# Optimization experiments

Measured on AMD Instinct MI355X. Metric: run time of the kernel, lower is better.

The kernel has to match this reference:

```python
import jax, jax.numpy as jnp
import numpy as np
from jax import lax

NMS_THRESH = 0.5
BN_EPS = 1e-5
TO_REMOVE = 1.0  # neural-motifs box convention (+1 in width/height)


def nms_overlaps(boxes):
    # boxes: [N, C, 4] xyxy -> per-class pairwise IoU [N, N, C]
    x1 = jnp.maximum(boxes[:, None, :, 0], boxes[None, :, :, 0])
    y1 = jnp.maximum(boxes[:, None, :, 1], boxes[None, :, :, 1])
    x2 = jnp.minimum(boxes[:, None, :, 2], boxes[None, :, :, 2])
    y2 = jnp.minimum(boxes[:, None, :, 3], boxes[None, :, :, 3])
    inter = jnp.clip(x2 - x1 + TO_REMOVE, 0.0) * jnp.clip(y2 - y1 + TO_REMOVE, 0.0)
    area = (boxes[:, :, 2] - boxes[:, :, 0] + TO_REMOVE) * (boxes[:, :, 3] - boxes[:, :, 1] + TO_REMOVE)  # [N,C]
    union = area[:, None, :] + area[None, :, :] - inter
    return inter / union


def greedy_nms_labels(obj_dists, is_overlap):
    # faithful port of nms_per_cls: iterative argmax + per-class suppression
    N, C = obj_dists.shape
    scores = jax.nn.softmax(obj_dists, axis=-1)
    scores = scores.at[:, 0].set(-1.0)  # kill background column

    def step(carry, _):
        scores, labels = carry
        flat = jnp.argmax(scores)          # row-major, same as np.unravel_index
        box_ind = flat // C
        cls_ind = flat % C
        labels = labels.at[box_ind].set(cls_ind.astype(jnp.int32))
        ov = is_overlap[box_ind, :, cls_ind]  # [N] bool
        col = jnp.where(ov, 0.0, scores[:, cls_ind])
        scores = scores.at[:, cls_ind].set(col)
        scores = scores.at[box_ind, :].set(-1.0)
        return (scores, labels), None

    (_, labels), _ = lax.scan(step, (scores, jnp.zeros(N, jnp.int32)), None, length=N)
    return labels


def setup_inputs() -> dict:
    key = jax.random.key(0)
    ks = jax.random.split(key, 16)
    N, C, D, E, H, P = 400, 151, 4096, 200, 512, 128
    x = jax.random.normal(ks[0], (N, D), jnp.float32)
    predict_logits = jax.random.normal(ks[1], (N, C), jnp.float32) * 2.0
    pos_input = jax.random.uniform(ks[2], (N, 9), jnp.float32)
    xy = jax.random.uniform(ks[3], (N, C, 2), jnp.float32) * 800.0
    wh = jax.random.uniform(ks[4], (N, C, 2), jnp.float32) * 200.0 + 1.0
    boxes_per_cls = jnp.concatenate([xy, xy + wh], axis=-1)
    sc = lambda k, sh: jax.random.normal(k, sh, jnp.float32) * np.float32(1.0 / np.sqrt(sh[0]))
    return {
        'x': x,
        'predict_logits': predict_logits,
        'pos_input': pos_input,
        'boxes_per_cls': boxes_per_cls,
        'obj_embed_w': jax.random.normal(ks[5], (C, E), jnp.float32) * 0.1,
        'obj_embed2_w': jax.random.normal(ks[6], (C, E), jnp.float32) * 0.1,
        'w_pos1': sc(ks[7], (9, 32)), 'b_pos1': jnp.zeros(32, jnp.float32),
        'bn_gamma': jnp.ones(32, jnp.float32), 'bn_beta': jnp.zeros(32, jnp.float32),
        'bn_mean': jnp.zeros(32, jnp.float32), 'bn_var': jnp.ones(32, jnp.float32),
        'w_pos2': sc(ks[8], (32, P)), 'b_pos2': jnp.zeros(P, jnp.float32),
        'w_lin': sc(ks[9], (D + E + P, H)), 'b_lin': jnp.zeros(H, jnp.float32),
        'w_out': sc(ks[10], (H, C)), 'b_out': jnp.zeros(C, jnp.float32),
        'w_fc': sc(ks[11], (D + E + P, H)), 'b_fc': jnp.zeros(H, jnp.float32),
    }


def reference(x, predict_logits, pos_input, boxes_per_cls, obj_embed_w, obj_embed2_w,
              w_pos1, b_pos1, bn_gamma, bn_beta, bn_mean, bn_var, w_pos2, b_pos2,
              w_lin, b_lin, w_out, b_out, w_fc, b_fc):
    # sgdet inference path of VTransEFeaturePE.forward
    obj_embed = jax.nn.softmax(predict_logits, axis=-1) @ obj_embed_w           # [N,E]
    h = pos_input @ w_pos1 + b_pos1                                             # Linear(9,32)
    h = (h - bn_mean) / jnp.sqrt(bn_var + BN_EPS) * bn_gamma + bn_beta          # BN eval
    pos_embed = jax.nn.relu(h @ w_pos2 + b_pos2)                                # [N,128]
    rep = jnp.concatenate([x, obj_embed, pos_embed], axis=-1)                   # [N,4424]
    obj_dists = (rep @ w_lin + b_lin) @ w_out + b_out                           # [N,C]
    is_overlap = nms_overlaps(boxes_per_cls) >= NMS_THRESH                      # [N,N,C]
    obj_preds = greedy_nms_labels(obj_dists, is_overlap)                        # [N] int32
    obj_embed2 = obj_embed2_w[obj_preds]                                        # [N,E]
    obj_rel_rep = jnp.concatenate([x, pos_embed, obj_embed2], axis=-1)
    edge_ctx = jax.nn.relu(obj_rel_rep @ w_fc + b_fc)                           # [N,H]
    return (obj_dists, obj_preds, edge_ctx)
```

## Files before the change

### kernel.cpp

```cpp
#include <hip/hip_runtime.h>
#include <hip/hip_bf16.h>
#include <stdint.h>

#define NB 400
#define NC 151
#define DX 4096
#define DE 200
#define DP 128
#define DH 512
#define KREP 4424
#define TAILW 328
#define MPAD 416
#define SPLITK 8
#define TILES1 139
#define TILES2 132
#define SKSTRIDE 152

__device__ __forceinline__ uint32_t f2ord(float f) {
  uint32_t u = __float_as_uint(f);
  return (u & 0x80000000u) ? ~u : (u | 0x80000000u);
}

__global__ __launch_bounds__(256) void k_embed(
    const float* __restrict__ logits, const float* __restrict__ obj_embed_w,
    const float* __restrict__ pos_input, const float* __restrict__ w_pos1,
    const float* __restrict__ b_pos1, const float* __restrict__ bn_gamma,
    const float* __restrict__ bn_beta, const float* __restrict__ bn_mean,
    const float* __restrict__ bn_var, const float* __restrict__ w_pos2,
    const float* __restrict__ b_pos2, float* __restrict__ tail1) {
  int r = blockIdx.x, t = threadIdx.x;
  if (r >= NB) {
    if (t < TAILW) tail1[r * TAILW + t] = 0.f;
    return;
  }
  __shared__ float p[NC];
  __shared__ float red[256];
  __shared__ float hb[32];

  float v = (t < NC) ? logits[r * NC + t] : -INFINITY;
  red[t] = v; __syncthreads();
  for (int s = 128; s > 0; s >>= 1) { if (t < s) red[t] = fmaxf(red[t], red[t + s]); __syncthreads(); }
  float m = red[0]; __syncthreads();
  float e = (t < NC) ? expf(v - m) : 0.f;
  red[t] = e; __syncthreads();
  for (int s = 128; s > 0; s >>= 1) { if (t < s) red[t] += red[t + s]; __syncthreads(); }
  float sum = red[0];
  if (t < NC) p[t] = e / sum;

  if (t < 32) {
    float acc = b_pos1[t];
    for (int k = 0; k < 9; k++) acc += pos_input[r * 9 + k] * w_pos1[k * 32 + t];
    acc = (acc - bn_mean[t]) / sqrtf(bn_var[t] + 1e-5f) * bn_gamma[t] + bn_beta[t];
    hb[t] = acc;
  }
  __syncthreads();

  if (t < DE) {
    float acc = 0.f;
    for (int k = 0; k < NC; k++) acc += p[k] * obj_embed_w[k * DE + t];
    tail1[r * TAILW + t] = acc;
  }
  if (t < DP) {
    float acc = b_pos2[t];
    for (int k = 0; k < 32; k++) acc += hb[k] * w_pos2[k * DP + t];
    tail1[r * TAILW + DE + t] = fmaxf(acc, 0.f);
  }
}

__device__ __forceinline__ void gemm_body(
    float (*As)[36], float (*Bs)[68],
    const float* __restrict__ x, const float* __restrict__ tail,
    const float* __restrict__ w, float* __restrict__ part,
    int bid, int tiles, int toff) {
  int tid = threadIdx.x;
  int n0 = (bid & 7) * 64, m0 = ((bid >> 3) % 13) * 32;
  int z = bid / 104;
  int tbeg = (z * tiles) / SPLITK, tend = ((z + 1) * tiles) / SPLITK;
  int ty = tid >> 4, tx = tid & 15;
  int a_r = tid >> 3, a_c = (tid & 7) << 2;
  int b_r = tid >> 4, b_c = (tid & 15) << 2;
  float4 acc0 = {0, 0, 0, 0}, acc1 = {0, 0, 0, 0};

  auto loadA = [&](int t) -> float4 {
    int k = t * 32 + a_c;
    int row = m0 + a_r;
    float4 v = {0, 0, 0, 0};
    if (k < KREP) {
      if (k < DX) { if (row < NB) v = *(const float4*)&x[(size_t)row * DX + k]; }
      else v = *(const float4*)&tail[row * TAILW + toff + (k - DX)];
    }
    return v;
  };
  auto loadB = [&](int t, int roff) -> float4 {
    int k = t * 32 + b_r + roff;
    float4 v = {0, 0, 0, 0};
    if (k < KREP) v = *(const float4*)&w[(size_t)k * DH + n0 + b_c];
    return v;
  };

  float4 pa = loadA(tbeg), pb0 = loadB(tbeg, 0), pb1 = loadB(tbeg, 16);
  for (int t = tbeg; t < tend; t++) {
    __syncthreads();
    *(float4*)&As[a_r][a_c] = pa;
    *(float4*)&Bs[b_r][b_c] = pb0;
    *(float4*)&Bs[b_r + 16][b_c] = pb1;
    __syncthreads();
    if (t + 1 < tend) { pa = loadA(t + 1); pb0 = loadB(t + 1, 0); pb1 = loadB(t + 1, 16); }
#pragma unroll
    for (int k4 = 0; k4 < 8; k4++) {
      float4 a0 = *(float4*)&As[ty * 2][k4 * 4];
      float4 a1 = *(float4*)&As[ty * 2 + 1][k4 * 4];
#pragma unroll
      for (int j = 0; j < 4; j++) {
        float4 bv = *(float4*)&Bs[k4 * 4 + j][tx * 4];
        float av0 = (&a0.x)[j], av1 = (&a1.x)[j];
        acc0.x += av0 * bv.x; acc0.y += av0 * bv.y; acc0.z += av0 * bv.z; acc0.w += av0 * bv.w;
        acc1.x += av1 * bv.x; acc1.y += av1 * bv.y; acc1.z += av1 * bv.z; acc1.w += av1 * bv.w;
      }
    }
  }
  int row0 = m0 + ty * 2, col = n0 + tx * 4;
  float* base = part + (size_t)z * NB * DH;
  if (row0 < NB)     *(float4*)&base[row0 * DH + col] = acc0;
  if (row0 + 1 < NB) *(float4*)&base[(row0 + 1) * DH + col] = acc1;
}

__global__ __launch_bounds__(256) void k_g1ov(
    const float* __restrict__ x, const float* __restrict__ tail1,
    const float* __restrict__ w_lin, float* __restrict__ part,
    const float* __restrict__ boxes, uint64_t* __restrict__ ov_bits) {
  __shared__ __align__(16) float As[32][36];
  __shared__ __align__(16) float Bs[32][68];
  int bid = blockIdx.x;
  if (bid >= 832) {
    int c = bid - 832;
    int t = threadIdx.x;
    __shared__ float4 bx[NB];
    const float4* bp4 = (const float4*)boxes;
    for (int j = t; j < NB; j += 256) bx[j] = bp4[j * NC + c];
    __syncthreads();
    int wave = t >> 6, lane = t & 63;
    for (int b = wave; b < NB; b += 4) {
      float4 A = bx[b];
      float areaA = (A.z - A.x + 1.f) * (A.w - A.y + 1.f);
      for (int chunk = 0; chunk < 7; chunk++) {
        int j = chunk * 64 + lane;
        bool ov = false;
        if (j < NB) {
          float4 B = bx[j];
          float x1 = fmaxf(A.x, B.x), y1 = fmaxf(A.y, B.y);
          float x2 = fminf(A.z, B.z), y2 = fminf(A.w, B.w);
          float iw = fmaxf(x2 - x1 + 1.f, 0.f), ih = fmaxf(y2 - y1 + 1.f, 0.f);
          float inter = iw * ih;
          float areaB = (B.z - B.x + 1.f) * (B.w - B.y + 1.f);
          ov = (inter / (areaA + areaB - inter)) >= 0.5f;
        }
        uint64_t mask = __ballot(ov);
        if (lane == 0) ov_bits[((size_t)(b * NC + c) << 3) + chunk] = mask;
      }
    }
    return;
  }
  gemm_body(As, Bs, x, tail1, w_lin, part, bid, TILES1, 0);
}

__global__ __launch_bounds__(256) void k_dists(
    const float* __restrict__ part, const float* __restrict__ b_lin,
    const float* __restrict__ w_out, const float* __restrict__ b_out,
    float* __restrict__ out_dists, uint64_t* __restrict__ skeys) {
  int r = blockIdx.x, t = threadIdx.x;
  __shared__ float h[DH];
  __shared__ float red[256];
  __shared__ float sval[NC];
  float s0 = b_lin[t], s1 = b_lin[t + 256];
#pragma unroll
  for (int z = 0; z < SPLITK; z++) {
    const float* pr = part + ((size_t)z * NB + r) * DH;
    s0 += pr[t]; s1 += pr[t + 256];
  }
  h[t] = s0; h[t + 256] = s1;
  __syncthreads();

  float acc = -INFINITY;
  if (t < NC) {
    acc = b_out[t];
    for (int k = 0; k < DH; k++) acc += h[k] * w_out[k * NC + t];
    out_dists[r * NC + t] = acc;
  }
  red[t] = (t < NC) ? acc : -INFINITY; __syncthreads();
  for (int s = 128; s > 0; s >>= 1) { if (t < s) red[t] = fmaxf(red[t], red[t + s]); __syncthreads(); }
  float mx = red[0]; __syncthreads();
  float e = (t < NC) ? expf(acc - mx) : 0.f;
  red[t] = e; __syncthreads();
  for (int s = 128; s > 0; s >>= 1) { if (t < s) red[t] += red[t + s]; __syncthreads(); }
  float sum = red[0];
  if (t < NC) sval[t] = e / sum;
  __syncthreads();

  if (t >= 1 && t < NC) {
    float v = sval[t];
    int rank = 0;
    for (int c2 = 1; c2 < NC; c2++) {
      float v2 = sval[c2];
      rank += (v2 > v) || (v2 == v && c2 < t);
    }
    skeys[(size_t)r * SKSTRIDE + rank] =
        ((uint64_t)f2ord(v) << 17) | ((uint64_t)(511 - r) << 8) | (uint64_t)t;
  }
}

struct GemmSm { float As[32][36]; float Bs[32][68]; };
struct NmsSm  { uint64_t top4[2][4][4]; uint64_t amask[8]; uint64_t rmask[8];
                uint8_t rcol[512]; };

__global__ __launch_bounds__(256) void k_nms_g2a(
    const uint64_t* __restrict__ ov_bits, const uint64_t* __restrict__ skeys,
    int* __restrict__ labels_g, float* __restrict__ out_preds,
    const float* __restrict__ x, const float* __restrict__ tail1,
    const float* __restrict__ w_fc, float* __restrict__ part) {
  __shared__ __align__(16) union { GemmSm g; NmsSm n; } sm;
  if (blockIdx.x > 0) {
    gemm_body(sm.g.As, sm.g.Bs, x, tail1, w_fc, part, blockIdx.x - 1, TILES2, DE);
    return;
  }
  int tid = threadIdx.x, wave = tid >> 6, lane = tid & 63;
  int S0w = wave * 2;
  uint64_t cand[2];
  uint64_t supp0[2], supp1[2], supp2[2];
  int depth[2];
  bool removed[2];
  int reszmin[2];

#pragma unroll
  for (int u = 0; u < 2; u++) {
    int r = (S0w + u) * 64 + lane;
    supp0[u] = supp1[u] = supp2[u] = 0;
    depth[u] = 0; removed[u] = false; reszmin[u] = 255;
    if (r < NB) {
      cand[u] = skeys[(size_t)r * SKSTRIDE];
      labels_g[r] = 0; out_preds[r] = 0.f;
    } else cand[u] = 0;
  }

  auto cswap = [](uint64_t& a, uint64_t& b) {
    uint64_t hi = a > b ? a : b, lo = a > b ? b : a; a = hi; b = lo;
  };

  int picked = 0, rr = 0;
  while (picked < NB) {
    int pp = rr & 1; rr++;
    uint64_t k0 = cand[0] > cand[1] ? cand[0] : cand[1];
    uint64_t k1 = cand[0] > cand[1] ? cand[1] : cand[0];
    uint64_t k2 = 0, k3 = 0;
#pragma unroll
    for (int off = 1; off < 64; off <<= 1) {
      uint64_t p0 = (uint64_t)__shfl_xor((unsigned long long)k0, off, 64);
      uint64_t p1 = (uint64_t)__shfl_xor((unsigned long long)k1, off, 64);
      uint64_t p2 = (uint64_t)__shfl_xor((unsigned long long)k2, off, 64);
      uint64_t p3 = (uint64_t)__shfl_xor((unsigned long long)k3, off, 64);
      uint64_t t0 = k0 > p3 ? k0 : p3;
      uint64_t t1 = k1 > p2 ? k1 : p2;
      uint64_t t2 = k2 > p1 ? k2 : p1;
      uint64_t t3 = k3 > p0 ? k3 : p0;
      cswap(t0, t2); cswap(t1, t3); cswap(t0, t1); cswap(t2, t3);
      k0 = t0; k1 = t1; k2 = t2; k3 = t3;
    }
    if (lane < 4) {
      uint64_t kv = (lane == 0) ? k0 : (lane == 1) ? k1 : (lane == 2) ? k2 : k3;
      sm.n.top4[pp][wave][lane] = kv;
    }
    __syncthreads();

    uint64_t A0 = sm.n.top4[pp][0][0], A1 = sm.n.top4[pp][0][1], A2 = sm.n.top4[pp][0][2], A3 = sm.n.top4[pp][0][3];
    uint64_t B0 = sm.n.top4[pp][1][0], B1 = sm.n.top4[pp][1][1], B2 = sm.n.top4[pp][1][2], B3 = sm.n.top4[pp][1][3];
    uint64_t C0 = sm.n.top4[pp][2][0], C1 = sm.n.top4[pp][2][1], C2 = sm.n.top4[pp][2][2], C3 = sm.n.top4[pp][2][3];
    uint64_t D0 = sm.n.top4[pp][3][0], D1 = sm.n.top4[pp][3][1], D2 = sm.n.top4[pp][3][2], D3 = sm.n.top4[pp][3][3];
    uint64_t x0 = A0, x1 = A1, x2 = A2, x3 = A3, x4 = B3, x5 = B2, x6 = B1, x7 = B0;
    cswap(x0,x4); cswap(x1,x5); cswap(x2,x6); cswap(x3,x7);
    cswap(x0,x2); cswap(x1,x3); cswap(x4,x6); cswap(x5,x7);
    cswap(x0,x1); cswap(x2,x3); cswap(x4,x5); cswap(x6,x7);
    uint64_t y0 = C0, y1 = C1, y2 = C2, y3 = C3, y4 = D3, y5 = D2, y6 = D1, y7 = D0;
    cswap(y0,y4); cswap(y1,y5); cswap(y2,y6); cswap(y3,y7);
    cswap(y0,y2); cswap(y1,y3); cswap(y4,y6); cswap(y5,y7);
    cswap(y0,y1); cswap(y2,y3); cswap(y4,y5); cswap(y6,y7);
    uint64_t tk[8];
    tk[0] = x0 > y7 ? x0 : y7;  tk[1] = x1 > y6 ? x1 : y6;
    tk[2] = x2 > y5 ? x2 : y5;  tk[3] = x3 > y4 ? x3 : y4;
    tk[4] = x4 > y3 ? x4 : y3;  tk[5] = x5 > y2 ? x5 : y2;
    tk[6] = x6 > y1 ? x6 : y1;  tk[7] = x7 > y0 ? x7 : y0;
    cswap(tk[0],tk[4]); cswap(tk[1],tk[5]); cswap(tk[2],tk[6]); cswap(tk[3],tk[7]);
    cswap(tk[0],tk[2]); cswap(tk[1],tk[3]); cswap(tk[4],tk[6]); cswap(tk[5],tk[7]);
    cswap(tk[0],tk[1]); cswap(tk[2],tk[3]); cswap(tk[4],tk[5]); cswap(tk[6],tk[7]);

    if ((uint32_t)(tk[0] >> 17) <= 0x80000000u) break;

    int cntA = 0, cntB = 0, cntC = 0, cntD = 0;
#pragma unroll
    for (int i = 0; i < 8; i++) {
      cntA += (tk[i] > A3); cntB += (tk[i] > B3);
      cntC += (tk[i] > C3); cntD += (tk[i] > D3);
    }
    int mincnt = cntA < cntB ? cntA : cntB;
    mincnt = mincnt < cntC ? mincnt : cntC;
    mincnt = mincnt < cntD ? mincnt : cntD;

    int npick = NB - picked; if (npick > 8) npick = 8;

    int pi = lane >> 3, pw = lane & 7;
    int bsel = 0, csel = 0;
#pragma unroll
    for (int i = 0; i < 8; i++)
      if (pi == i) {
        bsel = 511 - (int)((tk[i] >> 8) & 0x1FF);
        csel = (int)(tk[i] & 0xFF);
      }
    uint64_t wv = 0;
    if (pi < npick && pw < 7)
      wv = ov_bits[(((size_t)(bsel * NC + csel)) << 3) + pw];
    uint32_t packed = ((uint32_t)bsel << 8) | (uint32_t)csel;

    uint64_t balnz_raw = __ballot(wv != 0ull);

    uint64_t ovall = 0;
#pragma unroll
    for (int j = 0; j < 8; j++) {
      int bj = 511 - (int)((tk[j] >> 8) & 0x1FF);
      bool hit = (pw == (bj >> 6)) && ((wv >> (bj & 63)) & 1);
      uint64_t bal = __ballot(hit);
      bal |= bal >> 4; bal |= bal >> 2; bal |= bal >> 1;
      uint32_t m8 = (uint32_t)(((bal & 0x0101010101010101ULL) * 0x0102040810204080ULL) >> 56);
      ovall |= (uint64_t)m8 << (8 * j);
    }

    int napply = 1; bool stop = false;
#pragma unroll
    for (int j = 1; j < 8; j++) {
      bool bad = (j >= npick) || (j > mincnt) ||
                 ((uint32_t)(tk[j] >> 17) <= 0x80000000u);
      int cjv = (int)(tk[j] & 0xFF);
#pragma unroll
      for (int i = 0; i < j; i++)
        bad = bad || (((int)(tk[i] & 0xFF) == cjv) && ((ovall >> (8 * j + i)) & 1));
      stop = stop || bad;
      if (!stop) napply = j + 1;
    }

    uint64_t am = (napply >= 8) ? ~0ull : ((1ull << (8 * napply)) - 1);
    uint64_t balnz = balnz_raw & am;

#pragma unroll
    for (int u = 0; u < 2; u++) {
      int S = S0w + u;
      int r = S * 64 + lane;
      for (int i = 0; i < napply; i++) {
        int bc = __shfl((int)packed, i * 8, 64);
        int b = (bc >> 8) & 0x1FF, c = bc & 0xFF;
        bool act = ((balnz >> (i * 8 + S)) & 1) || ((b >> 6) == S);
        if (!act) continue;
        uint64_t owv = (uint64_t)__shfl((unsigned long long)wv, i * 8 + S, 64);
        if (r == b) {
          removed[u] = true; reszmin[u] = 255;
          cand[u] = ((uint64_t)0x407FFFFFu << 17) | ((uint64_t)(511 - r) << 8);
          labels_g[b] = c; out_preds[b] = (float)c;
        } else if ((owv >> lane) & 1) {
          if (removed[u]) {
            if (c < reszmin[u]) reszmin[u] = c;
            cand[u] = ((uint64_t)0x80000000u << 17) | ((uint64_t)(511 - r) << 8)
                      | (uint64_t)reszmin[u];
          } else {
            uint64_t bit = 1ull << (c & 63);
            if (c < 64) supp0[u] |= bit; else if (c < 128) supp1[u] |= bit; else supp2[u] |= bit;
            if ((int)(cand[u] & 0xFF) == c) {
              int d = depth[u] + 1;
              uint64_t k = 0;
              for (; d < 150; d++) {
                k = skeys[(size_t)r * SKSTRIDE + d];
                int col = (int)(k & 0xFF);
                uint64_t mm = (col < 64) ? supp0[u] : ((col < 128) ? supp1[u] : supp2[u]);
                if (!((mm >> (col & 63)) & 1)) break;
              }
              if (d >= 150)
                k = ((uint64_t)0x80000000u << 17) | ((uint64_t)(511 - r) << 8) | 1ull;
              depth[u] = d; cand[u] = k;
            }
          }
        }
      }
    }
    picked += napply;
  }

  if (picked < NB) {
#pragma unroll
    for (int u = 0; u < 2; u++) {
      int r = (S0w + u) * 64 + lane;
      uint64_t am = __ballot(r < NB && !removed[u]);
      uint64_t rm = __ballot(removed[u] &&
                             (uint32_t)(cand[u] >> 17) == 0x80000000u);
      sm.n.rcol[(S0w + u) * 64 + lane] = (uint8_t)reszmin[u];
      if (lane == 0) { sm.n.amask[S0w + u] = am; sm.n.rmask[S0w + u] = rm; }
    }
    __syncthreads();
    if (wave != 0) return;

    uint64_t A[8], R[8];
    uint32_t rc[8];
#pragma unroll
    for (int s = 0; s < 8; s++) {
      A[s] = sm.n.amask[s];
      R[s] = sm.n.rmask[s];
      rc[s] = sm.n.rcol[s * 64 + lane];
    }

    while (picked < NB) {
      int b = 0, sstar = 0; bool found = false;
#pragma unroll
      for (int s = 0; s < 8; s++) {
        uint64_t cm = A[s] | R[s];
        if (!found && cm != 0ull) {
          found = true; sstar = s;
          b = s * 64 + (int)__builtin_ctzll(cm);
        }
      }
      bool fromA = false;
      uint32_t colv = 0;
      if (found) {
#pragma unroll
        for (int s = 0; s < 8; s++)
          if (s == sstar) fromA = (A[s] >> (b & 63)) & 1ull;
        if (fromA) colv = 1;
        else {
          uint32_t cv = 0;
#pragma unroll
          for (int s = 0; s < 8; s++) {
            uint32_t v = (uint32_t)__shfl((int)rc[s], b & 63, 64);
            if (s == sstar) cv = v;
          }
          colv = cv;
        }
      }
      uint64_t w = 0;
      if (lane < 7) w = ov_bits[(((size_t)(b * NC + (int)colv)) << 3) + lane];
      uint64_t W[8];
#pragma unroll
      for (int s = 0; s < 8; s++)
        W[s] = (uint64_t)__shfl((unsigned long long)w, s, 64);
      uint64_t T[8];
#pragma unroll
      for (int s = 0; s < 8; s++) {
        uint64_t valid = (s < 6) ? ~0ull : ((s == 6) ? 0xFFFFull : 0ull);
        T[s] = W[s] & valid & ~A[s];
      }
#pragma unroll
      for (int s = 0; s < 8; s++)
        if (s == sstar) T[s] &= ~(1ull << (b & 63));
#pragma unroll
      for (int s = 0; s < 8; s++)
        if (s == sstar) {
          if (fromA) A[s] &= ~(1ull << (b & 63));
          else       R[s] &= ~(1ull << (b & 63));
        }
#pragma unroll
      for (int s = 0; s < 8; s++) {
        R[s] |= T[s];
        if ((T[s] >> lane) & 1ull) rc[s] = rc[s] < colv ? rc[s] : colv;
      }
      if (!fromA) {
#pragma unroll
        for (int s = 0; s < 8; s++)
          if (s == sstar && lane == (b & 63)) rc[s] = 255;
      }
      if (lane == 0) { labels_g[b] = (int)colv; out_preds[b] = (float)colv; }
      picked++;
    }
  }
}

__global__ __launch_bounds__(256) void k_final(
    const float* __restrict__ emb2, const int* __restrict__ labels,
    const float* __restrict__ w_fc, const float* __restrict__ part,
    const float* __restrict__ b_fc, float* __restrict__ out_edge) {
  __shared__ __align__(16) float As[32][36];
  __shared__ __align__(16) float Bs[32][68];
  int tid = threadIdx.x;
  int n0 = blockIdx.x * 64, m0 = blockIdx.y * 32;
  int ty = tid >> 4, tx = tid & 15;
  int a_r = tid >> 3, a_c = (tid & 7) << 2;
  int b_r = tid >> 4, b_c = (tid & 15) << 2;
  float4 acc0 = {0, 0, 0, 0}, acc1 = {0, 0, 0, 0};
  int row_a = m0 + a_r;
  int lab = (row_a < NB) ? labels[row_a] : 0;

  auto loadA = [&](int t) -> float4 {
    int kk = t * 32 + a_c;
    float4 v = {0, 0, 0, 0};
    if (kk < DE && row_a < NB) v = *(const float4*)&emb2[(size_t)lab * DE + kk];
    return v;
  };
  auto loadB = [&](int t, int roff) -> float4 {
    int kk = t * 32 + b_r + roff;
    float4 v = {0, 0, 0, 0};
    if (kk < DE) v = *(const float4*)&w_fc[(size_t)(DX + DP + kk) * DH + n0 + b_c];
    return v;
  };

  float4 pa = loadA(0), pb0 = loadB(0, 0), pb1 = loadB(0, 16);
  for (int t = 0; t < 7; t++) {
    __syncthreads();
    *(float4*)&As[a_r][a_c] = pa;
    *(float4*)&Bs[b_r][b_c] = pb0;
    *(float4*)&Bs[b_r + 16][b_c] = pb1;
    __syncthreads();
    if (t + 1 < 7) { pa = loadA(t + 1); pb0 = loadB(t + 1, 0); pb1 = loadB(t + 1, 16); }
#pragma unroll
    for (int k4 = 0; k4 < 8; k4++) {
      float4 a0 = *(float4*)&As[ty * 2][k4 * 4];
      float4 a1 = *(float4*)&As[ty * 2 + 1][k4 * 4];
#pragma unroll
      for (int j = 0; j < 4; j++) {
        float4 bv = *(float4*)&Bs[k4 * 4 + j][tx * 4];
        float av0 = (&a0.x)[j], av1 = (&a1.x)[j];
        acc0.x += av0 * bv.x; acc0.y += av0 * bv.y; acc0.z += av0 * bv.z; acc0.w += av0 * bv.w;
        acc1.x += av1 * bv.x; acc1.y += av1 * bv.y; acc1.z += av1 * bv.z; acc1.w += av1 * bv.w;
      }
    }
  }
  int row0 = m0 + ty * 2, col = n0 + tx * 4;
#pragma unroll
  for (int z = 0; z < SPLITK; z++) {
    if (row0 < NB) {
      float4 p = *(const float4*)&part[((size_t)z * NB + row0) * DH + col];
      acc0.x += p.x; acc0.y += p.y; acc0.z += p.z; acc0.w += p.w;
    }
    if (row0 + 1 < NB) {
      float4 p = *(const float4*)&part[((size_t)z * NB + row0 + 1) * DH + col];
      acc1.x += p.x; acc1.y += p.y; acc1.z += p.z; acc1.w += p.w;
    }
  }
  float4 bv = *(const float4*)&b_fc[col];
  if (row0 < NB) {
    float4 r;
    r.x = fmaxf(acc0.x + bv.x, 0.f); r.y = fmaxf(acc0.y + bv.y, 0.f);
    r.z = fmaxf(acc0.z + bv.z, 0.f); r.w = fmaxf(acc0.w + bv.w, 0.f);
    *(float4*)&out_edge[row0 * DH + col] = r;
  }
  if (row0 + 1 < NB) {
    float4 r;
    r.x = fmaxf(acc1.x + bv.x, 0.f); r.y = fmaxf(acc1.y + bv.y, 0.f);
    r.z = fmaxf(acc1.z + bv.z, 0.f); r.w = fmaxf(acc1.w + bv.w, 0.f);
    *(float4*)&out_edge[(row0 + 1) * DH + col] = r;
  }
}

extern "C" void kernel_launch(void* const* d_in, const int* in_sizes, int n_in,
                              void* d_out, int out_size, void* d_ws, size_t ws_size,
                              hipStream_t stream) {
  const float* x            = (const float*)d_in[0];
  const float* logits       = (const float*)d_in[1];
  const float* pos_input    = (const float*)d_in[2];
  const float* boxes        = (const float*)d_in[3];
  const float* obj_embed_w  = (const float*)d_in[4];
  const float* obj_embed2_w = (const float*)d_in[5];
  const float* w_pos1       = (const float*)d_in[6];
  const float* b_pos1       = (const float*)d_in[7];
  const float* bn_gamma     = (const float*)d_in[8];
  const float* bn_beta      = (const float*)d_in[9];
  const float* bn_mean      = (const float*)d_in[10];
  const float* bn_var       = (const float*)d_in[11];
  const float* w_pos2       = (const float*)d_in[12];
  const float* b_pos2       = (const float*)d_in[13];
  const float* w_lin        = (const float*)d_in[14];
  const float* b_lin        = (const float*)d_in[15];
  const float* w_out        = (const float*)d_in[16];
  const float* b_out        = (const float*)d_in[17];
  const float* w_fc         = (const float*)d_in[18];
  const float* b_fc         = (const float*)d_in[19];

  float* ws         = (float*)d_ws;
  float* tail1      = ws;
  int* labels       = (int*)(tail1 + MPAD * TAILW);
  uint64_t* skeys   = (uint64_t*)(labels + MPAD);
  uint64_t* ov_bits = skeys + (size_t)NB * SKSTRIDE;
  float* part       = (float*)(ov_bits + (size_t)NB * NC * 8);

  float* out       = (float*)d_out;
  float* out_dists = out;
  float* out_preds = out + NB * NC;
  float* out_edge  = out + NB * NC + NB;

  k_embed<<<MPAD, 256, 0, stream>>>(logits, obj_embed_w, pos_input, w_pos1, b_pos1,
                                    bn_gamma, bn_beta, bn_mean, bn_var, w_pos2, b_pos2,
                                    tail1);
  k_g1ov<<<983, 256, 0, stream>>>(x, tail1, w_lin, part, boxes, ov_bits);
  k_dists<<<NB, 256, 0, stream>>>(part, b_lin, w_out, b_out, out_dists, skeys);
  k_nms_g2a<<<833, 256, 0, stream>>>(ov_bits, skeys, labels, out_preds,
                                     x, tail1, w_fc, part);
  k_final<<<dim3(8, 13), 256, 0, stream>>>(obj_embed2_w, labels, w_fc, part,
                                           b_fc, out_edge);
}
```

Measured before the change: 566.5 us.

## Cache per-row overlap bitmasks in LDS for the serial NMS tail

Before the single-wave serial tail loop, the block preloads each remaining row's overlap bitmask row into shared memory, using class 1 or the row's recorded min suppressed class. The per-pick global load on the serial critical path becomes an LDS read. When a row's recorded class drops, its cached mask is refreshed from global memory inside the loop, per suppressed bit. This adds about 25KB of shared memory to the union and serial per-bit work, which may lower occupancy of the GEMM blocks sharing the kernel.

Result: no change. 567.5 us (+0.2%).

```diff
diff --git a/kernel.cpp b/kernel.cpp
--- a/kernel.cpp
+++ b/kernel.cpp
@@ -211,7 +211,7 @@
 
 struct GemmSm { float As[32][36]; float Bs[32][68]; };
 struct NmsSm  { uint64_t top4[2][4][4]; uint64_t amask[8]; uint64_t rmask[8];
-                uint8_t rcol[512]; };
+                uint32_t rcol32[512]; uint64_t ovc[NB][8]; };
 
 __global__ __launch_bounds__(256) void k_nms_g2a(
     const uint64_t* __restrict__ ov_bits, const uint64_t* __restrict__ skeys,
@@ -397,20 +397,28 @@
       uint64_t am = __ballot(r < NB && !removed[u]);
       uint64_t rm = __ballot(removed[u] &&
                              (uint32_t)(cand[u] >> 17) == 0x80000000u);
-      sm.n.rcol[(S0w + u) * 64 + lane] = (uint8_t)reszmin[u];
+      sm.n.rcol32[(S0w + u) * 64 + lane] = (uint32_t)reszmin[u];
       if (lane == 0) { sm.n.amask[S0w + u] = am; sm.n.rmask[S0w + u] = rm; }
     }
     __syncthreads();
+    for (int i = tid; i < NB * 8; i += 256) {
+      int r = i >> 3, w = i & 7;
+      sm.n.ovc[r][w] = (w < 7) ? ov_bits[(((size_t)(r * NC + 1)) << 3) + w] : 0;
+    }
+    __syncthreads();
+    for (int r = tid; r < NB; r += 256) {
+      if ((sm.n.rmask[r >> 6] >> (r & 63)) & 1ull) {
+        uint32_t c = sm.n.rcol32[r];
+        for (int w = 0; w < 7; w++)
+          sm.n.ovc[r][w] = ov_bits[(((size_t)(r * NC + (int)c)) << 3) + w];
+      }
+    }
+    __syncthreads();
     if (wave != 0) return;
 
     uint64_t A[8], R[8];
-    uint32_t rc[8];
-#pragma unroll
-    for (int s = 0; s < 8; s++) {
-      A[s] = sm.n.amask[s];
-      R[s] = sm.n.rmask[s];
-      rc[s] = sm.n.rcol[s * 64 + lane];
-    }
+#pragma unroll
+    for (int s = 0; s < 8; s++) { A[s] = sm.n.amask[s]; R[s] = sm.n.rmask[s]; }
 
     while (picked < NB) {
       int b = 0, sstar = 0; bool found = false;
@@ -423,28 +431,25 @@
         }
       }
       bool fromA = false;
+#pragma unroll
+      for (int s = 0; s < 8; s++)
+        if (s == sstar) fromA = (A[s] >> (b & 63)) & 1ull;
+      if (!found) fromA = false;
       uint32_t colv = 0;
+      if (found) colv = fromA ? 1u : sm.n.rcol32[b];
+
+      uint64_t W[8];
       if (found) {
 #pragma unroll
+        for (int s = 0; s < 7; s++) W[s] = sm.n.ovc[b][s];
+        W[7] = 0;
+      } else {
+        uint64_t w = 0;
+        if (lane < 7) w = ov_bits[(((size_t)(b * NC + (int)colv)) << 3) + lane];
+#pragma unroll
         for (int s = 0; s < 8; s++)
-          if (s == sstar) fromA = (A[s] >> (b & 63)) & 1ull;
-        if (fromA) colv = 1;
-        else {
-          uint32_t cv = 0;
-#pragma unroll
-          for (int s = 0; s < 8; s++) {
-            uint32_t v = (uint32_t)__shfl((int)rc[s], b & 63, 64);
-            if (s == sstar) cv = v;
-          }
-          colv = cv;
-        }
-      }
-      uint64_t w = 0;
-      if (lane < 7) w = ov_bits[(((size_t)(b * NC + (int)colv)) << 3) + lane];
-      uint64_t W[8];
-#pragma unroll
-      for (int s = 0; s < 8; s++)
-        W[s] = (uint64_t)__shfl((unsigned long long)w, s, 64);
+          W[s] = (uint64_t)__shfl((unsigned long long)w, s, 64);
+      }
       uint64_t T[8];
 #pragma unroll
       for (int s = 0; s < 8; s++) {
@@ -453,22 +458,35 @@
       }
 #pragma unroll
       for (int s = 0; s < 8; s++)
-        if (s == sstar) T[s] &= ~(1ull << (b & 63));
-#pragma unroll
-      for (int s = 0; s < 8; s++)
         if (s == sstar) {
-          if (fromA) A[s] &= ~(1ull << (b & 63));
-          else       R[s] &= ~(1ull << (b & 63));
+          T[s] &= ~(1ull << (b & 63));
+          if (found) {
+            if (fromA) A[s] &= ~(1ull << (b & 63));
+            else       R[s] &= ~(1ull << (b & 63));
+          }
         }
+      if (found && !fromA) {
+        if (lane == 0) sm.n.rcol32[b] = 255;
+      }
+#pragma unroll
+      for (int s = 0; s < 8; s++) R[s] |= T[s];
+
 #pragma unroll
       for (int s = 0; s < 8; s++) {
-        R[s] |= T[s];
-        if ((T[s] >> lane) & 1ull) rc[s] = rc[s] < colv ? rc[s] : colv;
-      }
-      if (!fromA) {
-#pragma unroll
-        for (int s = 0; s < 8; s++)
-          if (s == sstar && lane == (b & 63)) rc[s] = 255;
+        uint64_t tt = T[s];
+        while (tt) {
+          int bit = (int)__builtin_ctzll(tt); tt &= tt - 1;
+          int row = s * 64 + bit;
+          uint32_t rcv = sm.n.rcol32[row];
+          if (rcv > colv) {
+            if (lane == 0) sm.n.rcol32[row] = colv;
+            uint64_t w2 = 0;
+            if (lane < 7) {
+              w2 = ov_bits[(((size_t)(row * NC + (int)colv)) << 3) + lane];
+              sm.n.ovc[row][lane] = w2;
+            }
+          }
+        }
       }
       if (lane == 0) { labels_g[b] = (int)colv; out_preds[b] = (float)colv; }
       picked++;
```
